# Kernel optimization log

Hardware: AMD Instinct MI355X
Metric: run time of the kernel (lower is better)

The kernel has to match this reference:

```python
import jax, jax.numpy as jnp
import numpy as np

N_NODES = 50000
N_EDGES = 1600000
D = 128


def setup_inputs() -> dict:
    key = jax.random.key(0)
    k1, k2, k3, k4 = jax.random.split(key, 4)
    x = jax.random.normal(k1, (N_NODES, D), dtype=jnp.float32)
    edge_index = jax.random.randint(k2, (2, N_EDGES), 0, N_NODES, dtype=jnp.int64)
    # Xavier-uniform-like W; B is zeros in torch init but use small random for grad coverage
    limit = float(np.sqrt(6.0 / (D + D)))
    W = jax.random.uniform(k3, (D, D), dtype=jnp.float32, minval=-limit, maxval=limit)
    B = jax.random.uniform(k4, (D, D), dtype=jnp.float32, minval=-limit, maxval=limit)
    return {"x": x, "edge_index": edge_index, "W": W, "B": B}


def reference(x, edge_index, W, B):
    sources = edge_index[0]
    destinations = edge_index[1]
    # gather messages from source nodes, scatter-add into destinations
    messages = x[sources]  # [E, D]
    aggregated = jax.ops.segment_sum(messages, destinations, num_segments=N_NODES)  # [N, D]
    deg = jax.ops.segment_sum(jnp.ones((N_EDGES,), dtype=x.dtype), destinations, num_segments=N_NODES)
    deg = jnp.where(deg == 0, jnp.asarray(1.0, dtype=x.dtype), deg)
    mean_msg = aggregated / deg[:, None]
    # update: messages @ W.T + x @ B.T
    return mean_msg @ W.T + x @ B.T
```

## Files before the change

### kernel.cpp

```cpp
#include <hip/hip_runtime.h>
#include <hip/hip_bf16.h>

#define NN 50000
#define NE 1600000
#define DD 128
#define NPB 64
#define NBK 782
#define MAXB 2560
#define CHUNK 6144
#define NCB 261
#define WS 136

typedef __attribute__((ext_vector_type(8))) short short8;
typedef __attribute__((ext_vector_type(4))) float f32x4;

__device__ inline unsigned short to_bf16(float v) {
    __hip_bfloat16 h = __float2bfloat16(v);
    return __builtin_bit_cast(unsigned short, h);
}

__global__ __launch_bounds__(1024) void convscatter_k(const int* __restrict__ ei,
                                                      const float* __restrict__ x,
                                                      unsigned int* __restrict__ xb,
                                                      int* __restrict__ gcursor,
                                                      int* __restrict__ ebuf) {
    __shared__ int stg[CHUNK];
    __shared__ int h[NBK];
    __shared__ int lbase[NBK];
    __shared__ int gb[NBK];
    __shared__ int hcur[NBK];
    __shared__ int wsum[16], wbase[16];
    const int t = threadIdx.x;
    const int lane = t & 63, wv = t >> 6;
    const int e0 = blockIdx.x * CHUNK;
    const int ec = min(CHUNK, NE - e0);

    for (int i = t; i < NBK; i += 1024) h[i] = 0;
    __syncthreads();

    unsigned int w2[6];
    #pragma unroll
    for (int u = 0; u < 6; ++u) {
        int i = u * 1024 + t;
        if (i < ec) {
            int src = ei[e0 + i];
            int dst = ei[NE + e0 + i];
            int b = dst >> 6;
            w2[u] = ((unsigned)b << 22) | ((unsigned)src << 6) | (unsigned)(dst & 63);
            atomicAdd(&h[b], 1);
        } else w2[u] = 0xFFFFFFFFu;
    }

    {
        int gid = blockIdx.x * 1024 + t;
        const int total4 = NN * DD / 4;
        for (int i = gid; i < total4; i += NCB * 1024) {
            float4 v = ((const float4*)x)[i];
            int p = __builtin_amdgcn_cvt_pk_fp8_f32(v.x, v.y, 0, false);
            p = __builtin_amdgcn_cvt_pk_fp8_f32(v.z, v.w, p, true);
            xb[i] = (unsigned)p;
        }
    }
    __syncthreads();

    int v = (t < NBK) ? h[t] : 0;
    int s = v;
    #pragma unroll
    for (int o = 1; o < 64; o <<= 1) {
        int u = __shfl_up(s, o);
        if (lane >= o) s += u;
    }
    if (lane == 63) wsum[wv] = s;
    __syncthreads();
    if (wv == 0 && lane < 16) {
        int bv = wsum[lane];
        int bs = bv;
        #pragma unroll
        for (int o = 1; o < 16; o <<= 1) {
            int u = __shfl_up(bs, o);
            if (lane >= o) bs += u;
        }
        wbase[lane] = bs - bv;
    }
    __syncthreads();
    if (t < NBK) {
        int excl = s - v + wbase[wv];
        lbase[t] = excl;
        hcur[t] = excl;
        gb[t] = v ? t * MAXB + atomicAdd(&gcursor[t], v) : 0;
    }
    __syncthreads();

    #pragma unroll
    for (int u = 0; u < 6; ++u) {
        if (w2[u] != 0xFFFFFFFFu) {
            int b = w2[u] >> 22;
            int pos = atomicAdd(&hcur[b], 1);
            stg[pos] = (int)w2[u];
        }
    }
    __syncthreads();

    for (int i = t; i < ec; i += 1024) {
        unsigned int w = (unsigned)stg[i];
        int b = w >> 22;
        ebuf[gb[b] + (i - lbase[b])] = (int)(w & 0x3FFFFFu);
    }
}

__global__ __launch_bounds__(512) void sortagg_k(const unsigned int* __restrict__ xb,
                                                 const int* __restrict__ ebuf,
                                                 const int* __restrict__ gcursor,
                                                 unsigned int* __restrict__ meanb) {
    __shared__ int stg[MAXB];
    __shared__ unsigned short srt[MAXB];
    __shared__ int cnt8[8][NPB];
    __shared__ int cur[NPB], off[NPB + 1];
    const int b = blockIdx.x, t = threadIdx.x;
    const int wv = t >> 6, lane = t & 63;
    const int n = gcursor[b];
    const int* __restrict__ slab = ebuf + (size_t)b * MAXB;
    for (int i = t; i < n; i += 512) stg[i] = slab[i];
    if (lane < NPB) cnt8[wv][lane] = 0;
    __syncthreads();
    for (int i = t; i < n; i += 512) atomicAdd(&cnt8[wv][stg[i] & 63], 1);
    __syncthreads();
    if (t < 64) {
        int v = 0;
        #pragma unroll
        for (int w = 0; w < 8; ++w) v += cnt8[w][t];
        int s = v;
        #pragma unroll
        for (int o = 1; o < 64; o <<= 1) {
            int u = __shfl_up(s, o);
            if (t >= o) s += u;
        }
        cur[t] = s - v;
        off[t] = s - v;
        if (t == 63) off[64] = s;
    }
    __syncthreads();
    for (int i = t; i < n; i += 512) {
        int w = stg[i];
        int pos = atomicAdd(&cur[w & 63], 1);
        srt[pos] = (unsigned short)(w >> 6);
    }
    __syncthreads();

    const int half = lane >> 5, il = lane & 31;
    #pragma unroll
    for (int q = 0; q < 8; ++q) {
        int ln = wv + q * 8;
        int s0 = off[ln], s1 = off[ln + 1];
        float a0 = 0.f, a1 = 0.f, a2 = 0.f, a3 = 0.f;
        int i = s0;
        for (; i + 32 <= s1; i += 32) {
            unsigned int u[16];
            #pragma unroll
            for (int k = 0; k < 16; ++k)
                u[k] = xb[(size_t)srt[i + 2 * k + half] * 32 + il];
            #pragma unroll
            for (int k = 0; k < 16; ++k) {
                auto lo = __builtin_amdgcn_cvt_pk_f32_fp8((int)u[k], false);
                auto hi = __builtin_amdgcn_cvt_pk_f32_fp8((int)u[k], true);
                a0 += lo[0]; a1 += lo[1]; a2 += hi[0]; a3 += hi[1];
            }
        }
        if (i + 16 <= s1) {
            unsigned int u[8];
            #pragma unroll
            for (int k = 0; k < 8; ++k)
                u[k] = xb[(size_t)srt[i + 2 * k + half] * 32 + il];
            #pragma unroll
            for (int k = 0; k < 8; ++k) {
                auto lo = __builtin_amdgcn_cvt_pk_f32_fp8((int)u[k], false);
                auto hi = __builtin_amdgcn_cvt_pk_f32_fp8((int)u[k], true);
                a0 += lo[0]; a1 += lo[1]; a2 += hi[0]; a3 += hi[1];
            }
            i += 16;
        }
        for (; i < s1; i += 2) {
            int e = i + half;
            unsigned int u = (e < s1) ? xb[(size_t)srt[e] * 32 + il] : 0u;
            auto lo = __builtin_amdgcn_cvt_pk_f32_fp8((int)u, false);
            auto hi = __builtin_amdgcn_cvt_pk_f32_fp8((int)u, true);
            a0 += lo[0]; a1 += lo[1]; a2 += hi[0]; a3 += hi[1];
        }
        a0 += __shfl_xor(a0, 32);
        a1 += __shfl_xor(a1, 32);
        a2 += __shfl_xor(a2, 32);
        a3 += __shfl_xor(a3, 32);
        int node = b * NPB + ln;
        if (half == 0 && node < NN) {
            float inv = 1.0f / fmaxf((float)(s1 - s0), 1.0f);
            unsigned lo = (unsigned)to_bf16(a0 * inv) | ((unsigned)to_bf16(a1 * inv) << 16);
            unsigned hi = (unsigned)to_bf16(a2 * inv) | ((unsigned)to_bf16(a3 * inv) << 16);
            ((uint2*)meanb)[(size_t)node * 32 + il] = make_uint2(lo, hi);
        }
    }
}

__global__ __launch_bounds__(256) void gemm_mfma_k(const unsigned short* __restrict__ meanb,
                                                   const float* __restrict__ x,
                                                   const float* __restrict__ W,
                                                   const float* __restrict__ Bm,
                                                   float* __restrict__ out) {
    __shared__ unsigned short Wt[DD * WS];
    __shared__ unsigned short Bt[DD * WS];
    const int tid = threadIdx.x;
    #pragma unroll
    for (int it = 0; it < 16; ++it) {
        int idx = it * 256 + tid;
        int n = idx >> 5;
        int k0 = (idx & 31) * 4;
        float4 w4 = ((const float4*)W)[idx];
        float4 b4 = ((const float4*)Bm)[idx];
        ushort4 wp, bp;
        wp.x = to_bf16(w4.x); wp.y = to_bf16(w4.y); wp.z = to_bf16(w4.z); wp.w = to_bf16(w4.w);
        bp.x = to_bf16(b4.x); bp.y = to_bf16(b4.y); bp.z = to_bf16(b4.z); bp.w = to_bf16(b4.w);
        *(ushort4*)&Wt[n * WS + k0] = wp;
        *(ushort4*)&Bt[n * WS + k0] = bp;
    }
    __syncthreads();

    const int wave = tid >> 6;
    const int lane = tid & 63;
    const int m = lane & 15;
    const int quad = lane >> 4;
    const int rowA = min(blockIdx.x * 64 + wave * 16 + m, NN - 1);

    f32x4 acc[8];
    #pragma unroll
    for (int nt = 0; nt < 8; ++nt) acc[nt] = (f32x4){0.f, 0.f, 0.f, 0.f};

    #pragma unroll
    for (int t = 0; t < 4; ++t) {
        const int k8 = t * 32 + quad * 8;
        short8 mf = *(const short8*)&meanb[(size_t)rowA * DD + k8];
        float xv[8];
        {
            const float4* xq = (const float4*)&x[(size_t)rowA * DD + k8];
            float4 b0 = xq[0], b1 = xq[1];
            xv[0] = b0.x; xv[1] = b0.y; xv[2] = b0.z; xv[3] = b0.w;
            xv[4] = b1.x; xv[5] = b1.y; xv[6] = b1.z; xv[7] = b1.w;
        }
        short8 xh, xl;
        #pragma unroll
        for (int j = 0; j < 8; ++j) {
            unsigned short g = to_bf16(xv[j]);
            xh[j] = (short)g;
            xl[j] = (short)to_bf16(xv[j] - __uint_as_float((unsigned)g << 16));
        }
        #pragma unroll
        for (int nt = 0; nt < 8; ++nt) {
            int nrow = nt * 16 + m;
            short8 wf = *(const short8*)&Wt[nrow * WS + k8];
            short8 bf = *(const short8*)&Bt[nrow * WS + k8];
            acc[nt] = __builtin_amdgcn_mfma_f32_16x16x32_bf16(xl, bf, acc[nt], 0, 0, 0);
            acc[nt] = __builtin_amdgcn_mfma_f32_16x16x32_bf16(mf, wf, acc[nt], 0, 0, 0);
            acc[nt] = __builtin_amdgcn_mfma_f32_16x16x32_bf16(xh, bf, acc[nt], 0, 0, 0);
        }
    }

    const int rowD0 = blockIdx.x * 64 + wave * 16 + quad * 4;
    #pragma unroll
    for (int nt = 0; nt < 8; ++nt) {
        #pragma unroll
        for (int r = 0; r < 4; ++r) {
            int row = rowD0 + r;
            if (row < NN) out[(size_t)row * DD + nt * 16 + m] = acc[nt][r];
        }
    }
}

extern "C" void kernel_launch(void* const* d_in, const int* in_sizes, int n_in,
                              void* d_out, int out_size, void* d_ws, size_t ws_size,
                              hipStream_t stream) {
    const float* x  = (const float*)d_in[0];
    const int*   ei = (const int*)d_in[1];
    const float* W  = (const float*)d_in[2];
    const float* Bm = (const float*)d_in[3];
    float* out = (float*)d_out;

    unsigned int* meanb = (unsigned int*)d_ws;
    unsigned int* xb    = meanb + (size_t)NN * 64;
    int* ebuf     = (int*)(xb + (size_t)NN * 32);
    int* gcursor  = ebuf + (size_t)NBK * MAXB;

    hipMemsetAsync(gcursor, 0, NBK * sizeof(int), stream);
    convscatter_k<<<NCB, 1024, 0, stream>>>(ei, x, xb, gcursor, ebuf);
    sortagg_k<<<NBK, 512, 0, stream>>>(xb, ebuf, gcursor, meanb);
    gemm_mfma_k<<<(NN + 63) / 64, 256, 0, stream>>>((const unsigned short*)meanb, x, W, Bm, out);
}
```

Baseline: 155.7 us.

## Fuse aggregation and MFMA GEMM into one kernel with shared-memory mean tile

Merges the sort/aggregate kernel with the GEMM kernel, so each 64-node block writes its bf16 mean rows into shared memory and immediately runs the MFMA update, with 8 waves splitting the output columns. This removes the global round trip for the mean buffer and one kernel launch. The W/B bf16 conversion moves into the first kernel's last block, and the gather now loads 8 bytes per lane with four edges in flight per wave. The tradeoffs are more shared memory per block, weight fragments read from global/L2 instead of LDS, and fewer GEMM-specialized blocks.

Measured after the change: 173.6 us. +11.5%, slower.

```diff
diff --git a/kernel.cpp b/kernel.cpp
--- a/kernel.cpp
+++ b/kernel.cpp
@@ -9,7 +9,7 @@
 #define MAXB 2560
 #define CHUNK 6144
 #define NCB 261
-#define WS 136
+#define WSM 136
 
 typedef __attribute__((ext_vector_type(8))) short short8;
 typedef __attribute__((ext_vector_type(4))) float f32x4;
@@ -21,7 +21,11 @@
 
 __global__ __launch_bounds__(1024) void convscatter_k(const int* __restrict__ ei,
                                                       const float* __restrict__ x,
+                                                      const float* __restrict__ W,
+                                                      const float* __restrict__ Bm,
                                                       unsigned int* __restrict__ xb,
+                                                      unsigned short* __restrict__ Wbf,
+                                                      unsigned short* __restrict__ Bbf,
                                                       int* __restrict__ gcursor,
                                                       int* __restrict__ ebuf) {
     __shared__ int stg[CHUNK];
@@ -61,6 +65,17 @@
             xb[i] = (unsigned)p;
         }
     }
+    if (blockIdx.x == NCB - 1) {
+        for (int i = t; i < DD * DD / 4; i += 1024) {
+            float4 w4 = ((const float4*)W)[i];
+            float4 b4 = ((const float4*)Bm)[i];
+            ushort4 wp, bp;
+            wp.x = to_bf16(w4.x); wp.y = to_bf16(w4.y); wp.z = to_bf16(w4.z); wp.w = to_bf16(w4.w);
+            bp.x = to_bf16(b4.x); bp.y = to_bf16(b4.y); bp.z = to_bf16(b4.z); bp.w = to_bf16(b4.w);
+            ((ushort4*)Wbf)[i] = wp;
+            ((ushort4*)Bbf)[i] = bp;
+        }
+    }
     __syncthreads();
 
     int v = (t < NBK) ? h[t] : 0;
@@ -108,22 +123,39 @@
     }
 }
 
-__global__ __launch_bounds__(512) void sortagg_k(const unsigned int* __restrict__ xb,
-                                                 const int* __restrict__ ebuf,
-                                                 const int* __restrict__ gcursor,
-                                                 unsigned int* __restrict__ meanb) {
+#define ACC2(U)                                                              \
+    {                                                                        \
+        auto l0 = __builtin_amdgcn_cvt_pk_f32_fp8((int)(U).x, false);        \
+        auto h0 = __builtin_amdgcn_cvt_pk_f32_fp8((int)(U).x, true);         \
+        auto l1 = __builtin_amdgcn_cvt_pk_f32_fp8((int)(U).y, false);        \
+        auto h1 = __builtin_amdgcn_cvt_pk_f32_fp8((int)(U).y, true);         \
+        a0 += l0[0]; a1 += l0[1]; a2 += h0[0]; a3 += h0[1];                  \
+        a4 += l1[0]; a5 += l1[1]; a6 += h1[0]; a7 += h1[1];                  \
+    }
+
+__global__ __launch_bounds__(512) void fused_k(const unsigned int* __restrict__ xb,
+                                               const int* __restrict__ ebuf,
+                                               const int* __restrict__ gcursor,
+                                               const unsigned short* __restrict__ Wbf,
+                                               const unsigned short* __restrict__ Bbf,
+                                               const float* __restrict__ x,
+                                               float* __restrict__ out) {
     __shared__ int stg[MAXB];
     __shared__ unsigned short srt[MAXB];
     __shared__ int cnt8[8][NPB];
     __shared__ int cur[NPB], off[NPB + 1];
+    __shared__ unsigned short meanL[NPB * WSM];
     const int b = blockIdx.x, t = threadIdx.x;
     const int wv = t >> 6, lane = t & 63;
-    const int n = gcursor[b];
+    const int n = min(gcursor[b], MAXB);
     const int* __restrict__ slab = ebuf + (size_t)b * MAXB;
-    for (int i = t; i < n; i += 512) stg[i] = slab[i];
-    if (lane < NPB) cnt8[wv][lane] = 0;
-    __syncthreads();
-    for (int i = t; i < n; i += 512) atomicAdd(&cnt8[wv][stg[i] & 63], 1);
+
+    cnt8[wv][lane] = 0;
+    for (int i = t; i < n; i += 512) {
+        int v = slab[i];
+        stg[i] = v;
+        atomicAdd(&cnt8[wv][v & 63], 1);
+    }
     __syncthreads();
     if (t < 64) {
         int v = 0;
@@ -147,128 +179,105 @@
     }
     __syncthreads();
 
-    const int half = lane >> 5, il = lane & 31;
+    const int sub = lane >> 4, il2 = lane & 15;
     #pragma unroll
     for (int q = 0; q < 8; ++q) {
         int ln = wv + q * 8;
         int s0 = off[ln], s1 = off[ln + 1];
         float a0 = 0.f, a1 = 0.f, a2 = 0.f, a3 = 0.f;
+        float a4 = 0.f, a5 = 0.f, a6 = 0.f, a7 = 0.f;
         int i = s0;
         for (; i + 32 <= s1; i += 32) {
-            unsigned int u[16];
-            #pragma unroll
-            for (int k = 0; k < 16; ++k)
-                u[k] = xb[(size_t)srt[i + 2 * k + half] * 32 + il];
-            #pragma unroll
-            for (int k = 0; k < 16; ++k) {
-                auto lo = __builtin_amdgcn_cvt_pk_f32_fp8((int)u[k], false);
-                auto hi = __builtin_amdgcn_cvt_pk_f32_fp8((int)u[k], true);
-                a0 += lo[0]; a1 += lo[1]; a2 += hi[0]; a3 += hi[1];
-            }
-        }
-        if (i + 16 <= s1) {
-            unsigned int u[8];
+            uint2 u[8];
             #pragma unroll
             for (int k = 0; k < 8; ++k)
-                u[k] = xb[(size_t)srt[i + 2 * k + half] * 32 + il];
+                u[k] = ((const uint2*)xb)[(size_t)srt[i + 4 * k + sub] * 16 + il2];
             #pragma unroll
-            for (int k = 0; k < 8; ++k) {
-                auto lo = __builtin_amdgcn_cvt_pk_f32_fp8((int)u[k], false);
-                auto hi = __builtin_amdgcn_cvt_pk_f32_fp8((int)u[k], true);
-                a0 += lo[0]; a1 += lo[1]; a2 += hi[0]; a3 += hi[1];
-            }
+            for (int k = 0; k < 8; ++k) ACC2(u[k]);
+        }
+        if (i + 16 <= s1) {
+            uint2 u[4];
+            #pragma unroll
+            for (int k = 0; k < 4; ++k)
+                u[k] = ((const uint2*)xb)[(size_t)srt[i + 4 * k + sub] * 16 + il2];
+            #pragma unroll
+            for (int k = 0; k < 4; ++k) ACC2(u[k]);
             i += 16;
         }
-        for (; i < s1; i += 2) {
-            int e = i + half;
-            unsigned int u = (e < s1) ? xb[(size_t)srt[e] * 32 + il] : 0u;
-            auto lo = __builtin_amdgcn_cvt_pk_f32_fp8((int)u, false);
-            auto hi = __builtin_amdgcn_cvt_pk_f32_fp8((int)u, true);
-            a0 += lo[0]; a1 += lo[1]; a2 += hi[0]; a3 += hi[1];
-        }
-        a0 += __shfl_xor(a0, 32);
-        a1 += __shfl_xor(a1, 32);
-        a2 += __shfl_xor(a2, 32);
-        a3 += __shfl_xor(a3, 32);
-        int node = b * NPB + ln;
-        if (half == 0 && node < NN) {
-            float inv = 1.0f / fmaxf((float)(s1 - s0), 1.0f);
-            unsigned lo = (unsigned)to_bf16(a0 * inv) | ((unsigned)to_bf16(a1 * inv) << 16);
-            unsigned hi = (unsigned)to_bf16(a2 * inv) | ((unsigned)to_bf16(a3 * inv) << 16);
-            ((uint2*)meanb)[(size_t)node * 32 + il] = make_uint2(lo, hi);
-        }
-    }
-}
-
-__global__ __launch_bounds__(256) void gemm_mfma_k(const unsigned short* __restrict__ meanb,
-                                                   const float* __restrict__ x,
-                                                   const float* __restrict__ W,
-                                                   const float* __restrict__ Bm,
-                                                   float* __restrict__ out) {
-    __shared__ unsigned short Wt[DD * WS];
-    __shared__ unsigned short Bt[DD * WS];
-    const int tid = threadIdx.x;
-    #pragma unroll
-    for (int it = 0; it < 16; ++it) {
-        int idx = it * 256 + tid;
-        int n = idx >> 5;
-        int k0 = (idx & 31) * 4;
-        float4 w4 = ((const float4*)W)[idx];
-        float4 b4 = ((const float4*)Bm)[idx];
-        ushort4 wp, bp;
-        wp.x = to_bf16(w4.x); wp.y = to_bf16(w4.y); wp.z = to_bf16(w4.z); wp.w = to_bf16(w4.w);
-        bp.x = to_bf16(b4.x); bp.y = to_bf16(b4.y); bp.z = to_bf16(b4.z); bp.w = to_bf16(b4.w);
-        *(ushort4*)&Wt[n * WS + k0] = wp;
-        *(ushort4*)&Bt[n * WS + k0] = bp;
-    }
-    __syncthreads();
-
-    const int wave = tid >> 6;
-    const int lane = tid & 63;
-    const int m = lane & 15;
-    const int quad = lane >> 4;
-    const int rowA = min(blockIdx.x * 64 + wave * 16 + m, NN - 1);
-
-    f32x4 acc[8];
-    #pragma unroll
-    for (int nt = 0; nt < 8; ++nt) acc[nt] = (f32x4){0.f, 0.f, 0.f, 0.f};
-
-    #pragma unroll
-    for (int t = 0; t < 4; ++t) {
-        const int k8 = t * 32 + quad * 8;
-        short8 mf = *(const short8*)&meanb[(size_t)rowA * DD + k8];
+        for (; i < s1; i += 4) {
+            int e = i + sub;
+            uint2 u;
+            if (e < s1) u = ((const uint2*)xb)[(size_t)srt[e] * 16 + il2];
+            else { u.x = 0u; u.y = 0u; }
+            ACC2(u);
+        }
+        a0 += __shfl_xor(a0, 16); a0 += __shfl_xor(a0, 32);
+        a1 += __shfl_xor(a1, 16); a1 += __shfl_xor(a1, 32);
+        a2 += __shfl_xor(a2, 16); a2 += __shfl_xor(a2, 32);
+        a3 += __shfl_xor(a3, 16); a3 += __shfl_xor(a3, 32);
+        a4 += __shfl_xor(a4, 16); a4 += __shfl_xor(a4, 32);
+        a5 += __shfl_xor(a5, 16); a5 += __shfl_xor(a5, 32);
+        a6 += __shfl_xor(a6, 16); a6 += __shfl_xor(a6, 32);
+        a7 += __shfl_xor(a7, 16); a7 += __shfl_xor(a7, 32);
+        float inv = 1.0f / fmaxf((float)(s1 - s0), 1.0f);
+        if (lane < 16) {
+            short8 sv;
+            sv[0] = (short)to_bf16(a0 * inv); sv[1] = (short)to_bf16(a1 * inv);
+            sv[2] = (short)to_bf16(a2 * inv); sv[3] = (short)to_bf16(a3 * inv);
+            sv[4] = (short)to_bf16(a4 * inv); sv[5] = (short)to_bf16(a5 * inv);
+            sv[6] = (short)to_bf16(a6 * inv); sv[7] = (short)to_bf16(a7 * inv);
+            *(short8*)&meanL[ln * WSM + il2 * 8] = sv;
+        }
+    }
+    __syncthreads();
+
+    const int rt = wv >> 1, ch = wv & 1;
+    const int m = lane & 15, quad = lane >> 4;
+    const int rowA = min(b * 64 + rt * 16 + m, NN - 1);
+
+    short8 xh[4], xl[4];
+    #pragma unroll
+    for (int tt = 0; tt < 4; ++tt) {
+        int k8 = tt * 32 + quad * 8;
+        const float4* xq = (const float4*)&x[(size_t)rowA * DD + k8];
+        float4 b0 = xq[0], b1 = xq[1];
         float xv[8];
-        {
-            const float4* xq = (const float4*)&x[(size_t)rowA * DD + k8];
-            float4 b0 = xq[0], b1 = xq[1];
-            xv[0] = b0.x; xv[1] = b0.y; xv[2] = b0.z; xv[3] = b0.w;
-            xv[4] = b1.x; xv[5] = b1.y; xv[6] = b1.z; xv[7] = b1.w;
-        }
-        short8 xh, xl;
+        xv[0] = b0.x; xv[1] = b0.y; xv[2] = b0.z; xv[3] = b0.w;
+        xv[4] = b1.x; xv[5] = b1.y; xv[6] = b1.z; xv[7] = b1.w;
         #pragma unroll
         for (int j = 0; j < 8; ++j) {
             unsigned short g = to_bf16(xv[j]);
-            xh[j] = (short)g;
-            xl[j] = (short)to_bf16(xv[j] - __uint_as_float((unsigned)g << 16));
-        }
-        #pragma unroll
-        for (int nt = 0; nt < 8; ++nt) {
-            int nrow = nt * 16 + m;
-            short8 wf = *(const short8*)&Wt[nrow * WS + k8];
-            short8 bf = *(const short8*)&Bt[nrow * WS + k8];
-            acc[nt] = __builtin_amdgcn_mfma_f32_16x16x32_bf16(xl, bf, acc[nt], 0, 0, 0);
+            xh[tt][j] = (short)g;
+            xl[tt][j] = (short)to_bf16(xv[j] - __uint_as_float((unsigned)g << 16));
+        }
+    }
+
+    f32x4 acc[4];
+    #pragma unroll
+    for (int nt = 0; nt < 4; ++nt) acc[nt] = (f32x4){0.f, 0.f, 0.f, 0.f};
+
+    #pragma unroll
+    for (int tt = 0; tt < 4; ++tt) {
+        int k8 = tt * 32 + quad * 8;
+        short8 mf = *(const short8*)&meanL[(rt * 16 + m) * WSM + k8];
+        #pragma unroll
+        for (int nt = 0; nt < 4; ++nt) {
+            int nrow = ch * 64 + nt * 16 + m;
+            short8 wf = *(const short8*)&Wbf[(size_t)nrow * DD + k8];
+            short8 bf = *(const short8*)&Bbf[(size_t)nrow * DD + k8];
+            acc[nt] = __builtin_amdgcn_mfma_f32_16x16x32_bf16(xl[tt], bf, acc[nt], 0, 0, 0);
             acc[nt] = __builtin_amdgcn_mfma_f32_16x16x32_bf16(mf, wf, acc[nt], 0, 0, 0);
-            acc[nt] = __builtin_amdgcn_mfma_f32_16x16x32_bf16(xh, bf, acc[nt], 0, 0, 0);
-        }
-    }
-
-    const int rowD0 = blockIdx.x * 64 + wave * 16 + quad * 4;
-    #pragma unroll
-    for (int nt = 0; nt < 8; ++nt) {
+            acc[nt] = __builtin_amdgcn_mfma_f32_16x16x32_bf16(xh[tt], bf, acc[nt], 0, 0, 0);
+        }
+    }
+
+    const int rowD0 = b * 64 + rt * 16 + quad * 4;
+    #pragma unroll
+    for (int nt = 0; nt < 4; ++nt) {
         #pragma unroll
         for (int r = 0; r < 4; ++r) {
             int row = rowD0 + r;
-            if (row < NN) out[(size_t)row * DD + nt * 16 + m] = acc[nt][r];
+            if (row < NN) out[(size_t)row * DD + ch * 64 + nt * 16 + m] = acc[nt][r];
         }
     }
 }
@@ -282,13 +291,13 @@
     const float* Bm = (const float*)d_in[3];
     float* out = (float*)d_out;
 
-    unsigned int* meanb = (unsigned int*)d_ws;
-    unsigned int* xb    = meanb + (size_t)NN * 64;
-    int* ebuf     = (int*)(xb + (size_t)NN * 32);
-    int* gcursor  = ebuf + (size_t)NBK * MAXB;
+    unsigned int* xb     = (unsigned int*)d_ws;
+    int* ebuf            = (int*)(xb + (size_t)NN * 32);
+    unsigned short* Wbf  = (unsigned short*)(ebuf + (size_t)NBK * MAXB);
+    unsigned short* Bbf  = Wbf + DD * DD;
+    int* gcursor         = (int*)(Bbf + DD * DD);
 
     hipMemsetAsync(gcursor, 0, NBK * sizeof(int), stream);
-    convscatter_k<<<NCB, 1024, 0, stream>>>(ei, x, xb, gcursor, ebuf);
-    sortagg_k<<<NBK, 512, 0, stream>>>(xb, ebuf, gcursor, meanb);
-    gemm_mfma_k<<<(NN + 63) / 64, 256, 0, stream>>>((const unsigned short*)meanb, x, W, Bm, out);
+    convscatter_k<<<NCB, 1024, 0, stream>>>(ei, x, W, Bm, xb, Wbf, Bbf, gcursor, ebuf);
+    fused_k<<<NBK, 512, 0, stream>>>(xb, ebuf, gcursor, Wbf, Bbf, x, out);
 }
```
